# Optimization experiments

Hardware: AMD Instinct MI355X
Metric: run time of the kernel (lower is better)

Reference implementation:

```python
import jax, jax.numpy as jnp
import numpy as np

H = 512
TEMPERATURE = 1.0


def setup_inputs() -> dict:
    key = jax.random.key(0)
    ks = jax.random.split(key, 9)
    B, Q, S = 4, 64, 1024
    scale = 1.0 / np.sqrt(H)
    return {
        "query": jax.random.normal(ks[0], (B, Q, H), jnp.float32),
        "key_": jax.random.normal(ks[1], (B, S, H), jnp.float32),
        "value": jax.random.normal(ks[2], (B, S, H), jnp.float32),
        "Wq": jax.random.normal(ks[3], (H, H), jnp.float32) * scale,
        "bq": jax.random.normal(ks[4], (H,), jnp.float32) * 0.01,
        "Wk": jax.random.normal(ks[5], (H, H), jnp.float32) * scale,
        "bk": jax.random.normal(ks[6], (H,), jnp.float32) * 0.01,
        "we": jax.random.normal(ks[7], (H,), jnp.float32) * scale,
        "be": jax.random.normal(ks[8], (), jnp.float32) * 0.01,
    }


def reference(query, key_, value, Wq, bq, Wk, bk, we, be):
    # query: [B,Q,H], key_/value: [B,S,H]
    qp = jnp.einsum("bqd,dh->bqh", query, Wq) + bq          # [B,Q,H]
    kp = jnp.einsum("bsd,dh->bsh", key_, Wk) + bk           # [B,S,H]
    attn_sum = jnp.tanh(qp[:, :, None, :] + kp[:, None, :, :])  # [B,Q,S,H]
    scores = (jnp.einsum("bqsh,h->bqs", attn_sum, we) + be) / TEMPERATURE
    weights = jax.nn.softmax(scores, axis=-1)               # [B,Q,S]
    context = jnp.einsum("bqs,bsh->bqh", weights, value)    # [B,Q,H]
    return context, weights
```

## Files before the change

kernel.cpp:

```cpp
#include <hip/hip_runtime.h>


constexpr int kB = 4;
constexpr int kQ = 64;
constexpr int kS = 1024;
constexpr int kH = 512;

typedef short bf16x8 __attribute__((ext_vector_type(8)));
typedef float f32x4 __attribute__((ext_vector_type(4)));

__device__ __forceinline__ unsigned bf16rtn_bits(float x) {
  unsigned u = __float_as_uint(x);
  u += 0x7FFFu + ((u >> 16) & 1u);
  return u;
}

__device__ __forceinline__ void glds16(const void* g, void* l) {
  __builtin_amdgcn_global_load_lds(
      (__attribute__((address_space(1))) void*)(g),
      (__attribute__((address_space(3))) void*)(l), 16, 0, 0);
}

__global__ __launch_bounds__(256) void convert_all(
    const float* __restrict__ Wk, const float* __restrict__ Wq,
    const float* __restrict__ key_, const float* __restrict__ query,
    unsigned short* __restrict__ Bhi, unsigned short* __restrict__ Blo,
    unsigned short* __restrict__ Xhi, unsigned short* __restrict__ Xlo) {
  __shared__ __align__(16) unsigned short LHi[128 * 40];
  __shared__ __align__(16) unsigned short LLo[128 * 40];
  const int bid = blockIdx.x;
  const int t = threadIdx.x;
  if (bid < 256) {
    const int gid = bid * 256 + t;
    const int c = gid & 63;
    const int g = (gid >> 6) & 3;
    const int kt = (gid >> 8) & 15;
    const int ct = (gid >> 12) & 7;
    const int mat = gid >> 15;
    const float* W = mat ? Wq : Wk;
    const float* src = W + (size_t)(kt * 32 + g * 8) * kH + ct * 64 + c;
    bf16x8 hv, lv;
#pragma unroll
    for (int j = 0; j < 8; j++) {
      float x = src[(size_t)j * kH];
      unsigned u = bf16rtn_bits(x);
      float hf = __uint_as_float(u & 0xFFFF0000u);
      unsigned v = bf16rtn_bits(x - hf);
      hv[j] = (short)(u >> 16);
      lv[j] = (short)(v >> 16);
    }
    *(bf16x8*)(Bhi + (size_t)gid * 8) = hv;
    *(bf16x8*)(Blo + (size_t)gid * 8) = lv;
    return;
  }
  const int xb = bid - 256;
  const int kt = xb & 15;
  const int rt = xb >> 4;
  const float* X = (rt < 32) ? (key_ + (size_t)rt * 128 * kH)
                             : (query + (size_t)(rt - 32) * 128 * kH);
  const int r = t >> 1, c0 = (t & 1) * 16;
  const float* src = X + (size_t)r * kH + kt * 32 + c0;
  bf16x8 hv0, hv1, lv0, lv1;
#pragma unroll
  for (int i = 0; i < 16; i++) {
    float x = src[i];
    unsigned u = bf16rtn_bits(x);
    float hf = __uint_as_float(u & 0xFFFF0000u);
    unsigned v = bf16rtn_bits(x - hf);
    if (i < 8) { hv0[i] = (short)(u >> 16); lv0[i] = (short)(v >> 16); }
    else       { hv1[i - 8] = (short)(u >> 16); lv1[i - 8] = (short)(v >> 16); }
  }
  *(bf16x8*)&LHi[r * 40 + c0] = hv0;
  *(bf16x8*)&LHi[r * 40 + c0 + 8] = hv1;
  *(bf16x8*)&LLo[r * 40 + c0] = lv0;
  *(bf16x8*)&LLo[r * 40 + c0 + 8] = lv1;
  __syncthreads();
  const size_t obase = (size_t)(rt * 16 + kt) * 512 * 8;
#pragma unroll
  for (int p = 0; p < 2; p++) {
    const int s = t + p * 256;
    const int rr = s & 127, g = s >> 7;
    *(uint4*)(Xhi + obase + (size_t)s * 8) = *(const uint4*)&LHi[rr * 40 + g * 8];
    *(uint4*)(Xlo + obase + (size_t)s * 8) = *(const uint4*)&LLo[rr * 40 + g * 8];
  }
}

__global__ __launch_bounds__(256) void proj_mfma(
    const unsigned short* __restrict__ Xhi, const unsigned short* __restrict__ Xlo,
    const unsigned short* __restrict__ Bhi, const unsigned short* __restrict__ Blo,
    const float* __restrict__ bk, const float* __restrict__ bq,
    float* __restrict__ Ek, float* __restrict__ Eq) {
  __shared__ __align__(16) unsigned short AhiL[2][2048];
  __shared__ __align__(16) unsigned short AloL[2][2048];
  __shared__ __align__(16) unsigned short BhiL[2][2048];
  __shared__ __align__(16) unsigned short BloL[2][2048];

  const int bid = blockIdx.y * 8 + blockIdx.x;
  int ct, rt;
  if (bid < 512) {
    ct = (bid >> 3) & 7;
    rt = (bid & 7) + 8 * (bid >> 6);
  } else {
    const int tb = bid - 512;
    ct = tb >> 2;
    rt = 64 + (tb & 3);
  }

  const int mat = (rt >= 64) ? 1 : 0;
  const float* bias = mat ? bq : bk;
  float* Y = mat ? (Eq + (size_t)(rt - 64) * 64 * kH)
                 : (Ek + (size_t)rt * 64 * kH);

  const int t = threadIdx.x;
  const int rt128 = rt >> 1, hhalf = rt & 1;
  const int ga_slot = ((t >> 6) << 7) + (hhalf << 6) + (t & 63);
  const unsigned short* gah = Xhi + ((size_t)(rt128 * 16) * 512 + ga_slot) * 8;
  const unsigned short* gal = Xlo + ((size_t)(rt128 * 16) * 512 + ga_slot) * 8;
  const unsigned short* gbh = Bhi + (((size_t)(mat * 8 + ct) * 16) * 256 + t) * 8;
  const unsigned short* gbl = Blo + (((size_t)(mat * 8 + ct) * 16) * 256 + t) * 8;

  auto stage = [&](int buf, int kt2) {
    glds16(gah + (size_t)kt2 * 512 * 8, &AhiL[buf][t * 8]);
    glds16(gal + (size_t)kt2 * 512 * 8, &AloL[buf][t * 8]);
    glds16(gbh + (size_t)kt2 * 256 * 8, &BhiL[buf][t * 8]);
    glds16(gbl + (size_t)kt2 * 256 * 8, &BloL[buf][t * 8]);
  };

  const int l = t & 63, lg = l >> 4, lr = l & 15;
  const int wv = t >> 6, wm = wv >> 1, wn = wv & 1;
  const int oa0 = (lg * 64 + wm * 32 + lr) * 8;
  const int ob0 = (lg * 64 + wn * 32 + lr) * 8;

  f32x4 acc[2][2];
#pragma unroll
  for (int m = 0; m < 2; m++)
#pragma unroll
    for (int n = 0; n < 2; n++) acc[m][n] = {0.f, 0.f, 0.f, 0.f};

  stage(0, 0);
  __syncthreads();

  int buf = 0;
  for (int kt2 = 0; kt2 < 16; kt2++) {
    if (kt2 < 15) stage(buf ^ 1, kt2 + 1);

    const unsigned short* Ah = AhiL[buf];
    const unsigned short* Al = AloL[buf];
    const unsigned short* Bh = BhiL[buf];
    const unsigned short* Bl = BloL[buf];
    bf16x8 ah[2], al[2], bh[2], bl[2];
#pragma unroll
    for (int m = 0; m < 2; m++) {
      ah[m] = *(const bf16x8*)(Ah + oa0 + m * 128);
      al[m] = *(const bf16x8*)(Al + oa0 + m * 128);
    }
#pragma unroll
    for (int n = 0; n < 2; n++) {
      bh[n] = *(const bf16x8*)(Bh + ob0 + n * 128);
      bl[n] = *(const bf16x8*)(Bl + ob0 + n * 128);
    }
#pragma unroll
    for (int m = 0; m < 2; m++)
#pragma unroll
      for (int n = 0; n < 2; n++) {
        acc[m][n] = __builtin_amdgcn_mfma_f32_16x16x32_bf16(ah[m], bh[n], acc[m][n], 0, 0, 0);
        acc[m][n] = __builtin_amdgcn_mfma_f32_16x16x32_bf16(al[m], bh[n], acc[m][n], 0, 0, 0);
        acc[m][n] = __builtin_amdgcn_mfma_f32_16x16x32_bf16(ah[m], bl[n], acc[m][n], 0, 0, 0);
      }

    __syncthreads();
    buf ^= 1;
  }

  const int col0 = ct * 64 + wn * 32 + lr;
  const float b0 = bias[col0];
  const float b1 = bias[col0 + 16];
#pragma unroll
  for (int m = 0; m < 2; m++) {
    const int row0 = wm * 32 + m * 16 + lg * 4;
#pragma unroll
    for (int jj = 0; jj < 4; jj++) {
      float* y = Y + (size_t)(row0 + jj) * kH;
      y[col0]      = __expf(2.f * (acc[m][0][jj] + b0));
      y[col0 + 16] = __expf(2.f * (acc[m][1][jj] + b1));
    }
  }
}

__global__ __launch_bounds__(256) void score_kernel(
    const float* __restrict__ Eq, const float* __restrict__ Ek,
    const float* __restrict__ we, float* __restrict__ sraw) {
  __shared__ __align__(16) float EkL[2][64 * 64];

  const int qt = blockIdx.x, st = blockIdx.y, b = blockIdx.z;
  const int t = threadIdx.x, lane = t & 63;
  const int wvu = __builtin_amdgcn_readfirstlane(t >> 6);
  const int s0 = st * 64;
  const int q0g = b * kQ + qt * 8;
  const int qA = wvu * 2;

  const float4* we4 = (const float4*)we;
  float4 u0 = we4[lane * 2], u1 = we4[lane * 2 + 1];
  float wsum = u0.x + u0.y + u0.z + u0.w + u1.x + u1.y + u1.z + u1.w;
#pragma unroll
  for (int off = 32; off; off >>= 1) wsum += __shfl_xor(wsum, off);

  const float4* qa4 = (const float4*)(Eq + (size_t)(q0g + qA) * kH);
  const float4* qb4 = (const float4*)(Eq + (size_t)(q0g + qA + 1) * kH);

  const int er = t >> 4;
  const int ej = t & 15;
  const float* ekg = Ek + (size_t)(b * kS + s0 + er) * kH + ej * 4;
  float4 pk[4];
  auto gload = [&](int c) {
#pragma unroll
    for (int i = 0; i < 4; i++)
      pk[i] = *(const float4*)(ekg + (size_t)(16 * i) * kH + c * 64);
  };
  auto lwrite = [&](int buf) {
#pragma unroll
    for (int i = 0; i < 4; i++) {
      const int row = er + 16 * i;
      *(float4*)(&EkL[buf][row * 64 + ((ej ^ (row & 15)) << 2)]) = pk[i];
    }
  };

  gload(0);
  lwrite(0);
  __syncthreads();

  float accA = 0.f, accB = 0.f;
  const int sw = lane & 15;

  for (int c = 0; c < 8; c++) {
    if (c < 7) gload(c + 1);
    const float* ekb = &EkL[c & 1][lane * 64];
#pragma unroll 4
    for (int g = 0; g < 16; g++) {
      float4 ek = *(const float4*)(ekb + ((g ^ sw) << 2));
      float4 w = we4[c * 16 + g];
      float4 qa = qa4[c * 16 + g];
      float4 qb = qb4[c * 16 + g];
      {
        float a1 = fmaf(qa.x, ek.x, 1.f), b1 = fmaf(qa.y, ek.y, 1.f);
        float n1 = fmaf(w.y, a1, w.x * b1);
        accA = fmaf(n1, __builtin_amdgcn_rcpf(a1 * b1), accA);
        float a2 = fmaf(qa.z, ek.z, 1.f), b2 = fmaf(qa.w, ek.w, 1.f);
        float n2 = fmaf(w.w, a2, w.z * b2);
        accA = fmaf(n2, __builtin_amdgcn_rcpf(a2 * b2), accA);
      }
      {
        float a1 = fmaf(qb.x, ek.x, 1.f), b1 = fmaf(qb.y, ek.y, 1.f);
        float n1 = fmaf(w.y, a1, w.x * b1);
        accB = fmaf(n1, __builtin_amdgcn_rcpf(a1 * b1), accB);
        float a2 = fmaf(qb.z, ek.z, 1.f), b2 = fmaf(qb.w, ek.w, 1.f);
        float n2 = fmaf(w.w, a2, w.z * b2);
        accB = fmaf(n2, __builtin_amdgcn_rcpf(a2 * b2), accB);
      }
    }
    if (c < 7) {
      __syncthreads();
      lwrite((c + 1) & 1);
      __syncthreads();
    }
  }

  sraw[(size_t)(q0g + qA + 0) * kS + s0 + lane] = fmaf(-2.f, accA, wsum);
  sraw[(size_t)(q0g + qA + 1) * kS + s0 + lane] = fmaf(-2.f, accB, wsum);
}

__global__ __launch_bounds__(256) void ctx_fused(
    const float* __restrict__ sraw, const float* __restrict__ value,
    float* __restrict__ wout, float* __restrict__ ctx) {
  __shared__ __align__(16) float wt[4][1024];
  __shared__ __align__(16) float parts[4][4][128];
  const int bid = blockIdx.x;
  const int qc = bid >> 4, b = (bid >> 2) & 3, hc = bid & 3;
  const int t = threadIdx.x, wv = t >> 6, lane = t & 63;
  const int grow = b * kQ + qc * 4 + wv;

  const float4* row4 = (const float4*)(sraw + (size_t)grow * kS);
  float4 v[4];
#pragma unroll
  for (int j = 0; j < 4; j++) v[j] = row4[lane + 64 * j];
  float m = -1e30f;
#pragma unroll
  for (int j = 0; j < 4; j++)
    m = fmaxf(m, fmaxf(fmaxf(v[j].x, v[j].y), fmaxf(v[j].z, v[j].w)));
#pragma unroll
  for (int off = 32; off; off >>= 1) m = fmaxf(m, __shfl_xor(m, off));
  float sum = 0.f;
#pragma unroll
  for (int j = 0; j < 4; j++) {
    v[j].x = __expf(v[j].x - m); v[j].y = __expf(v[j].y - m);
    v[j].z = __expf(v[j].z - m); v[j].w = __expf(v[j].w - m);
    sum += v[j].x + v[j].y + v[j].z + v[j].w;
  }
#pragma unroll
  for (int off = 32; off; off >>= 1) sum += __shfl_xor(sum, off);
  const float inv = 1.f / sum;
  float4* wrow = (float4*)&wt[wv][0];
  float4* gw = (float4*)(wout + (size_t)grow * kS);
#pragma unroll
  for (int j = 0; j < 4; j++) {
    v[j].x *= inv; v[j].y *= inv; v[j].z *= inv; v[j].w *= inv;
    wrow[lane + 64 * j] = v[j];
    if (hc == 0) gw[lane + 64 * j] = v[j];
  }
  __syncthreads();

  const float* vbase =
      value + ((size_t)b * kS + wv * 256) * kH + hc * 128 + lane * 2;
  float2 acc[4];
#pragma unroll
  for (int q = 0; q < 4; q++) acc[q] = {0.f, 0.f};
#pragma unroll 2
  for (int s4 = 0; s4 < 64; s4++) {
    float4 wq[4];
#pragma unroll
    for (int q = 0; q < 4; q++)
      wq[q] = *(const float4*)&wt[q][wv * 256 + s4 * 4];
#pragma unroll
    for (int u = 0; u < 4; u++) {
      const float2 vv = *(const float2*)(vbase + (size_t)(s4 * 4 + u) * kH);
      const float w0 = ((const float*)&wq[0])[u];
      const float w1 = ((const float*)&wq[1])[u];
      const float w2 = ((const float*)&wq[2])[u];
      const float w3 = ((const float*)&wq[3])[u];
      acc[0].x = fmaf(w0, vv.x, acc[0].x); acc[0].y = fmaf(w0, vv.y, acc[0].y);
      acc[1].x = fmaf(w1, vv.x, acc[1].x); acc[1].y = fmaf(w1, vv.y, acc[1].y);
      acc[2].x = fmaf(w2, vv.x, acc[2].x); acc[2].y = fmaf(w2, vv.y, acc[2].y);
      acc[3].x = fmaf(w3, vv.x, acc[3].x); acc[3].y = fmaf(w3, vv.y, acc[3].y);
    }
  }
#pragma unroll
  for (int q = 0; q < 4; q++)
    *(float2*)&parts[wv][q][lane * 2] = acc[q];
  __syncthreads();

  const int q = t >> 6, hp = t & 63;
  float2 r = {0.f, 0.f};
#pragma unroll
  for (int w = 0; w < 4; w++) {
    const float2 p2 = *(const float2*)&parts[w][q][hp * 2];
    r.x += p2.x; r.y += p2.y;
  }
  *(float2*)(ctx + (size_t)(b * kQ + qc * 4 + q) * kH + hc * 128 + hp * 2) = r;
}

extern "C" void kernel_launch(void* const* d_in, const int* in_sizes, int n_in,
                              void* d_out, int out_size, void* d_ws,
                              size_t ws_size, hipStream_t stream) {
  const float* query = (const float*)d_in[0];
  const float* key_  = (const float*)d_in[1];
  const float* value = (const float*)d_in[2];
  const float* Wq    = (const float*)d_in[3];
  const float* bq    = (const float*)d_in[4];
  const float* Wk    = (const float*)d_in[5];
  const float* bk    = (const float*)d_in[6];
  const float* we    = (const float*)d_in[7];

  float* ctx  = (float*)d_out;
  float* wout = (float*)d_out + (size_t)kB * kQ * kH;

  float* Eq = (float*)d_ws;
  float* Ek = Eq + (size_t)kB * kQ * kH;
  unsigned short* Bhi =
      (unsigned short*)((char*)d_ws + (size_t)(kB * kQ * kH + kB * kS * kH) * 4);
  unsigned short* Blo = Bhi + (size_t)2 * 8 * 16 * 256 * 8;
  unsigned short* Xhi = Blo + (size_t)2 * 8 * 16 * 256 * 8;
  unsigned short* Xlo = Xhi + (size_t)34 * 16 * 512 * 8;
  float* sraw = (float*)(Xlo + (size_t)34 * 16 * 512 * 8);

  convert_all<<<800, 256, 0, stream>>>(Wk, Wq, key_, query, Bhi, Blo, Xhi, Xlo);
  proj_mfma<<<dim3(8, 68), 256, 0, stream>>>(Xhi, Xlo, Bhi, Blo, bk, bq, Ek, Eq);
  score_kernel<<<dim3(8, 16, 4), 256, 0, stream>>>(Eq, Ek, we, sraw);
  ctx_fused<<<256, 256, 0, stream>>>(sraw, value, wout, ctx);
}
```

Before: 149.3 us.

## Transpose Ek output, split score over H quarters, triple-buffer projection GEMM

After: 139.1 us. 6.8% less time.

```diff
diff --git a/kernel.cpp b/kernel.cpp
--- a/kernel.cpp
+++ b/kernel.cpp
@@ -89,11 +89,12 @@
     const unsigned short* __restrict__ Xhi, const unsigned short* __restrict__ Xlo,
     const unsigned short* __restrict__ Bhi, const unsigned short* __restrict__ Blo,
     const float* __restrict__ bk, const float* __restrict__ bq,
-    float* __restrict__ Ek, float* __restrict__ Eq) {
-  __shared__ __align__(16) unsigned short AhiL[2][2048];
-  __shared__ __align__(16) unsigned short AloL[2][2048];
-  __shared__ __align__(16) unsigned short BhiL[2][2048];
-  __shared__ __align__(16) unsigned short BloL[2][2048];
+    float* __restrict__ EkT, float* __restrict__ Eq) {
+  __shared__ __align__(16) unsigned short AhiL[3][2048];
+  __shared__ __align__(16) unsigned short AloL[3][2048];
+  __shared__ __align__(16) unsigned short BhiL[3][2048];
+  __shared__ __align__(16) unsigned short BloL[3][2048];
+  __shared__ __align__(16) float T[64][65];
 
   const int bid = blockIdx.y * 8 + blockIdx.x;
   int ct, rt;
@@ -108,8 +109,6 @@
 
   const int mat = (rt >= 64) ? 1 : 0;
   const float* bias = mat ? bq : bk;
-  float* Y = mat ? (Eq + (size_t)(rt - 64) * 64 * kH)
-                 : (Ek + (size_t)rt * 64 * kH);
 
   const int t = threadIdx.x;
   const int rt128 = rt >> 1, hhalf = rt & 1;
@@ -138,16 +137,20 @@
     for (int n = 0; n < 2; n++) acc[m][n] = {0.f, 0.f, 0.f, 0.f};
 
   stage(0, 0);
-  __syncthreads();
-
-  int buf = 0;
+  stage(1, 1);
+
+#pragma unroll
   for (int kt2 = 0; kt2 < 16; kt2++) {
-    if (kt2 < 15) stage(buf ^ 1, kt2 + 1);
-
-    const unsigned short* Ah = AhiL[buf];
-    const unsigned short* Al = AloL[buf];
-    const unsigned short* Bh = BhiL[buf];
-    const unsigned short* Bl = BloL[buf];
+    if (kt2 < 15) asm volatile("s_waitcnt vmcnt(4)" ::: "memory");
+    else          asm volatile("s_waitcnt vmcnt(0)" ::: "memory");
+    __builtin_amdgcn_s_barrier();
+    __builtin_amdgcn_sched_barrier(0);
+
+    const int rb = kt2 % 3;
+    const unsigned short* Ah = AhiL[rb];
+    const unsigned short* Al = AloL[rb];
+    const unsigned short* Bh = BhiL[rb];
+    const unsigned short* Bl = BloL[rb];
     bf16x8 ah[2], al[2], bh[2], bl[2];
 #pragma unroll
     for (int m = 0; m < 2; m++) {
@@ -159,6 +162,7 @@
       bh[n] = *(const bf16x8*)(Bh + ob0 + n * 128);
       bl[n] = *(const bf16x8*)(Bl + ob0 + n * 128);
     }
+    if (kt2 < 14) stage((kt2 + 2) % 3, kt2 + 2);
 #pragma unroll
     for (int m = 0; m < 2; m++)
 #pragma unroll
@@ -167,110 +171,96 @@
         acc[m][n] = __builtin_amdgcn_mfma_f32_16x16x32_bf16(al[m], bh[n], acc[m][n], 0, 0, 0);
         acc[m][n] = __builtin_amdgcn_mfma_f32_16x16x32_bf16(ah[m], bl[n], acc[m][n], 0, 0, 0);
       }
-
-    __syncthreads();
-    buf ^= 1;
-  }
-
-  const int col0 = ct * 64 + wn * 32 + lr;
+    __builtin_amdgcn_sched_barrier(0);
+  }
+
+  const int colL = wn * 32 + lr;
+  const int col0 = ct * 64 + colL;
   const float b0 = bias[col0];
   const float b1 = bias[col0 + 16];
-#pragma unroll
-  for (int m = 0; m < 2; m++) {
-    const int row0 = wm * 32 + m * 16 + lg * 4;
-#pragma unroll
-    for (int jj = 0; jj < 4; jj++) {
-      float* y = Y + (size_t)(row0 + jj) * kH;
-      y[col0]      = __expf(2.f * (acc[m][0][jj] + b0));
-      y[col0 + 16] = __expf(2.f * (acc[m][1][jj] + b1));
-    }
-  }
-}
-
-__global__ __launch_bounds__(256) void score_kernel(
-    const float* __restrict__ Eq, const float* __restrict__ Ek,
-    const float* __restrict__ we, float* __restrict__ sraw) {
-  __shared__ __align__(16) float EkL[2][64 * 64];
-
-  const int qt = blockIdx.x, st = blockIdx.y, b = blockIdx.z;
+
+  if (mat == 0) {
+#pragma unroll
+    for (int m = 0; m < 2; m++) {
+      const int row0 = wm * 32 + m * 16 + lg * 4;
+#pragma unroll
+      for (int jj = 0; jj < 4; jj++) {
+        T[row0 + jj][colL]      = __expf(2.f * (acc[m][0][jj] + b0));
+        T[row0 + jj][colL + 16] = __expf(2.f * (acc[m][1][jj] + b1));
+      }
+    }
+    __syncthreads();
+    const int sl = t & 63;
+    const int cb = (t >> 6) * 16;
+    const int R = rt * 64 + sl;
+    const int bb = R >> 10, ss = R & 1023;
+    float* outp = EkT + ((size_t)(bb * kH + ct * 64)) * kS + ss;
+#pragma unroll
+    for (int i = 0; i < 16; i++)
+      outp[(size_t)(cb + i) * kS] = T[sl][cb + i];
+  } else {
+    float* Y = Eq + (size_t)(rt - 64) * 64 * kH;
+#pragma unroll
+    for (int m = 0; m < 2; m++) {
+      const int row0 = wm * 32 + m * 16 + lg * 4;
+#pragma unroll
+      for (int jj = 0; jj < 4; jj++) {
+        float* y = Y + (size_t)(row0 + jj) * kH;
+        y[col0]      = __expf(2.f * (acc[m][0][jj] + b0));
+        y[col0 + 16] = __expf(2.f * (acc[m][1][jj] + b1));
+      }
+    }
+  }
+}
+
+__global__ __launch_bounds__(128) void score_kernel(
+    const float* __restrict__ Eq, const float* __restrict__ EkT,
+    const float* __restrict__ we, float* __restrict__ sraw4) {
   const int t = threadIdx.x, lane = t & 63;
   const int wvu = __builtin_amdgcn_readfirstlane(t >> 6);
-  const int s0 = st * 64;
-  const int q0g = b * kQ + qt * 8;
-  const int qA = wvu * 2;
-
-  const float4* we4 = (const float4*)we;
-  float4 u0 = we4[lane * 2], u1 = we4[lane * 2 + 1];
-  float wsum = u0.x + u0.y + u0.z + u0.w + u1.x + u1.y + u1.z + u1.w;
-#pragma unroll
-  for (int off = 32; off; off >>= 1) wsum += __shfl_xor(wsum, off);
-
-  const float4* qa4 = (const float4*)(Eq + (size_t)(q0g + qA) * kH);
-  const float4* qb4 = (const float4*)(Eq + (size_t)(q0g + qA + 1) * kH);
-
-  const int er = t >> 4;
-  const int ej = t & 15;
-  const float* ekg = Ek + (size_t)(b * kS + s0 + er) * kH + ej * 4;
-  float4 pk[4];
-  auto gload = [&](int c) {
-#pragma unroll
-    for (int i = 0; i < 4; i++)
-      pk[i] = *(const float4*)(ekg + (size_t)(16 * i) * kH + c * 64);
-  };
-  auto lwrite = [&](int buf) {
-#pragma unroll
-    for (int i = 0; i < 4; i++) {
-      const int row = er + 16 * i;
-      *(float4*)(&EkL[buf][row * 64 + ((ej ^ (row & 15)) << 2)]) = pk[i];
-    }
-  };
-
-  gload(0);
-  lwrite(0);
-  __syncthreads();
-
-  float accA = 0.f, accB = 0.f;
-  const int sw = lane & 15;
-
-  for (int c = 0; c < 8; c++) {
-    if (c < 7) gload(c + 1);
-    const float* ekb = &EkL[c & 1][lane * 64];
+  const int u = blockIdx.x * 2 + wvu;
+  const int hq = u & 3, st = (u >> 2) & 15, qp = (u >> 6) & 31, b = u >> 11;
+  const int s = st * 64 + lane;
+  const int q0g = b * kQ + qp * 2;
+  const int h0 = hq * 128;
+
+  const float4* w4 = (const float4*)(we + h0);
+  const float4* qa4 = (const float4*)(Eq + (size_t)q0g * kH + h0);
+  const float4* qb4 = (const float4*)(Eq + (size_t)(q0g + 1) * kH + h0);
+  const float* ek = EkT + ((size_t)(b * kH + h0)) * kS + s;
+
+  float accA = 0.f, accB = 0.f, wsum = 0.f;
 #pragma unroll 4
-    for (int g = 0; g < 16; g++) {
-      float4 ek = *(const float4*)(ekb + ((g ^ sw) << 2));
-      float4 w = we4[c * 16 + g];
-      float4 qa = qa4[c * 16 + g];
-      float4 qb = qb4[c * 16 + g];
-      {
-        float a1 = fmaf(qa.x, ek.x, 1.f), b1 = fmaf(qa.y, ek.y, 1.f);
-        float n1 = fmaf(w.y, a1, w.x * b1);
-        accA = fmaf(n1, __builtin_amdgcn_rcpf(a1 * b1), accA);
-        float a2 = fmaf(qa.z, ek.z, 1.f), b2 = fmaf(qa.w, ek.w, 1.f);
-        float n2 = fmaf(w.w, a2, w.z * b2);
-        accA = fmaf(n2, __builtin_amdgcn_rcpf(a2 * b2), accA);
-      }
-      {
-        float a1 = fmaf(qb.x, ek.x, 1.f), b1 = fmaf(qb.y, ek.y, 1.f);
-        float n1 = fmaf(w.y, a1, w.x * b1);
-        accB = fmaf(n1, __builtin_amdgcn_rcpf(a1 * b1), accB);
-        float a2 = fmaf(qb.z, ek.z, 1.f), b2 = fmaf(qb.w, ek.w, 1.f);
-        float n2 = fmaf(w.w, a2, w.z * b2);
-        accB = fmaf(n2, __builtin_amdgcn_rcpf(a2 * b2), accB);
-      }
-    }
-    if (c < 7) {
-      __syncthreads();
-      lwrite((c + 1) & 1);
-      __syncthreads();
-    }
-  }
-
-  sraw[(size_t)(q0g + qA + 0) * kS + s0 + lane] = fmaf(-2.f, accA, wsum);
-  sraw[(size_t)(q0g + qA + 1) * kS + s0 + lane] = fmaf(-2.f, accB, wsum);
+  for (int g = 0; g < 32; g++) {
+    const float4 w = w4[g];
+    const float4 qa = qa4[g];
+    const float4 qb = qb4[g];
+    const float e0 = ek[(size_t)(4 * g + 0) * kS];
+    const float e1 = ek[(size_t)(4 * g + 1) * kS];
+    const float e2 = ek[(size_t)(4 * g + 2) * kS];
+    const float e3 = ek[(size_t)(4 * g + 3) * kS];
+    wsum += w.x + w.y + w.z + w.w;
+    {
+      float a1 = fmaf(qa.x, e0, 1.f), c1 = fmaf(qa.y, e1, 1.f);
+      accA = fmaf(fmaf(w.y, a1, w.x * c1), __builtin_amdgcn_rcpf(a1 * c1), accA);
+      float a2 = fmaf(qa.z, e2, 1.f), c2 = fmaf(qa.w, e3, 1.f);
+      accA = fmaf(fmaf(w.w, a2, w.z * c2), __builtin_amdgcn_rcpf(a2 * c2), accA);
+    }
+    {
+      float a1 = fmaf(qb.x, e0, 1.f), c1 = fmaf(qb.y, e1, 1.f);
+      accB = fmaf(fmaf(w.y, a1, w.x * c1), __builtin_amdgcn_rcpf(a1 * c1), accB);
+      float a2 = fmaf(qb.z, e2, 1.f), c2 = fmaf(qb.w, e3, 1.f);
+      accB = fmaf(fmaf(w.w, a2, w.z * c2), __builtin_amdgcn_rcpf(a2 * c2), accB);
+    }
+  }
+
+  float* plane = sraw4 + (size_t)hq * kB * kQ * kS;
+  plane[(size_t)(q0g + 0) * kS + s] = fmaf(-2.f, accA, wsum);
+  plane[(size_t)(q0g + 1) * kS + s] = fmaf(-2.f, accB, wsum);
 }
 
 __global__ __launch_bounds__(256) void ctx_fused(
-    const float* __restrict__ sraw, const float* __restrict__ value,
+    const float* __restrict__ sraw4, const float* __restrict__ value,
     float* __restrict__ wout, float* __restrict__ ctx) {
   __shared__ __align__(16) float wt[4][1024];
   __shared__ __align__(16) float parts[4][4][128];
@@ -279,10 +269,21 @@
   const int t = threadIdx.x, wv = t >> 6, lane = t & 63;
   const int grow = b * kQ + qc * 4 + wv;
 
-  const float4* row4 = (const float4*)(sraw + (size_t)grow * kS);
+  const size_t plane = (size_t)kB * kQ * kS / 4;
+  const float4* r0 = (const float4*)(sraw4) + (size_t)grow * (kS / 4);
+  const float4* r1 = r0 + plane;
+  const float4* r2 = r1 + plane;
+  const float4* r3 = r2 + plane;
   float4 v[4];
 #pragma unroll
-  for (int j = 0; j < 4; j++) v[j] = row4[lane + 64 * j];
+  for (int j = 0; j < 4; j++) {
+    const int idx = lane + 64 * j;
+    float4 p0 = r0[idx], p1 = r1[idx], p2 = r2[idx], p3 = r3[idx];
+    v[j].x = (p0.x + p1.x) + (p2.x + p3.x);
+    v[j].y = (p0.y + p1.y) + (p2.y + p3.y);
+    v[j].z = (p0.z + p1.z) + (p2.z + p3.z);
+    v[j].w = (p0.w + p1.w) + (p2.w + p3.w);
+  }
   float m = -1e30f;
 #pragma unroll
   for (int j = 0; j < 4; j++)
@@ -321,12 +322,12 @@
     for (int q = 0; q < 4; q++)
       wq[q] = *(const float4*)&wt[q][wv * 256 + s4 * 4];
 #pragma unroll
-    for (int u = 0; u < 4; u++) {
-      const float2 vv = *(const float2*)(vbase + (size_t)(s4 * 4 + u) * kH);
-      const float w0 = ((const float*)&wq[0])[u];
-      const float w1 = ((const float*)&wq[1])[u];
-      const float w2 = ((const float*)&wq[2])[u];
-      const float w3 = ((const float*)&wq[3])[u];
+    for (int uu = 0; uu < 4; uu++) {
+      const float2 vv = *(const float2*)(vbase + (size_t)(s4 * 4 + uu) * kH);
+      const float w0 = ((const float*)&wq[0])[uu];
+      const float w1 = ((const float*)&wq[1])[uu];
+      const float w2 = ((const float*)&wq[2])[uu];
+      const float w3 = ((const float*)&wq[3])[uu];
       acc[0].x = fmaf(w0, vv.x, acc[0].x); acc[0].y = fmaf(w0, vv.y, acc[0].y);
       acc[1].x = fmaf(w1, vv.x, acc[1].x); acc[1].y = fmaf(w1, vv.y, acc[1].y);
       acc[2].x = fmaf(w2, vv.x, acc[2].x); acc[2].y = fmaf(w2, vv.y, acc[2].y);
@@ -363,17 +364,17 @@
   float* ctx  = (float*)d_out;
   float* wout = (float*)d_out + (size_t)kB * kQ * kH;
 
-  float* Eq = (float*)d_ws;
-  float* Ek = Eq + (size_t)kB * kQ * kH;
+  float* Eq    = (float*)d_ws;
+  float* sraw4 = Eq + (size_t)kB * kQ * kH;
   unsigned short* Bhi =
       (unsigned short*)((char*)d_ws + (size_t)(kB * kQ * kH + kB * kS * kH) * 4);
   unsigned short* Blo = Bhi + (size_t)2 * 8 * 16 * 256 * 8;
   unsigned short* Xhi = Blo + (size_t)2 * 8 * 16 * 256 * 8;
   unsigned short* Xlo = Xhi + (size_t)34 * 16 * 512 * 8;
-  float* sraw = (float*)(Xlo + (size_t)34 * 16 * 512 * 8);
+  float* EkT = (float*)(Xlo + (size_t)34 * 16 * 512 * 8);
 
   convert_all<<<800, 256, 0, stream>>>(Wk, Wq, key_, query, Bhi, Blo, Xhi, Xlo);
-  proj_mfma<<<dim3(8, 68), 256, 0, stream>>>(Xhi, Xlo, Bhi, Blo, bk, bq, Ek, Eq);
-  score_kernel<<<dim3(8, 16, 4), 256, 0, stream>>>(Eq, Ek, we, sraw);
-  ctx_fused<<<256, 256, 0, stream>>>(sraw, value, wout, ctx);
-}
+  proj_mfma<<<dim3(8, 68), 256, 0, stream>>>(Xhi, Xlo, Bhi, Blo, bk, bq, EkT, Eq);
+  score_kernel<<<4096, 128, 0, stream>>>(Eq, EkT, we, sraw4);
+  ctx_fused<<<256, 256, 0, stream>>>(sraw4, value, wout, ctx);
+}
```
